# Kernel optimization log

Measured on AMD Instinct MI355X. Metric: run time of the kernel, lower is better.

Reference implementation:

```python
import jax, jax.numpy as jnp
import numpy as np

N_GRAPHS = 512
NODES_PER_G = 200
EDGES_PER_G = 6400
N = N_GRAPHS * NODES_PER_G        # 102400 nodes
E = N_GRAPHS * EDGES_PER_G        # 3276800 edges
HID = 128
NCLS = 10


def _linear_params(key, fan_in, fan_out):
    # torch nn.Linear default init: U(-1/sqrt(fan_in), 1/sqrt(fan_in))
    s = 1.0 / np.sqrt(fan_in)
    kw, kb = jax.random.split(key)
    W = jax.random.uniform(kw, (fan_in, fan_out), minval=-s, maxval=s, dtype=jnp.float32)
    b = jax.random.uniform(kb, (fan_out,), minval=-s, maxval=s, dtype=jnp.float32)
    return W, b


def setup_inputs() -> dict:
    key = jax.random.key(0)
    ks = jax.random.split(key, 10)
    # edges are confined within each graph (DGL batched graph structure)
    g_off = (jnp.arange(E, dtype=jnp.int32) // EDGES_PER_G) * NODES_PER_G
    src = (g_off + jax.random.randint(ks[0], (E,), 0, NODES_PER_G)).astype(jnp.int32)
    dst = (g_off + jax.random.randint(ks[1], (E,), 0, NODES_PER_G)).astype(jnp.int32)
    W1, b1 = _linear_params(ks[2], 1, HID)
    W2, b2 = _linear_params(ks[3], HID, HID)
    Wa, ba = _linear_params(ks[4], HID, 512)
    Wb, bb = _linear_params(ks[5], 512, 1024)
    Wc, bc = _linear_params(ks[6], 1024, 1024)
    Wd, bd = _linear_params(ks[7], 1024, 512)
    We, be = _linear_params(ks[8], 512, NCLS)
    return dict(src=src, dst=dst, W1=W1, b1=b1, W2=W2, b2=b2,
                Wa=Wa, ba=ba, Wb=Wb, bb=bb, Wc=Wc, bc=bc,
                Wd=Wd, bd=bd, We=We, be=be)


def reference(src, dst, W1, b1, W2, b2, Wa, ba, Wb, bb, Wc, bc, Wd, bd, We, be):
    seg = jax.ops.segment_sum
    ones = jnp.ones((E,), jnp.float32)
    in_deg = seg(ones, dst, num_segments=N)    # [N]
    out_deg = seg(ones, src, num_segments=N)   # [N]
    # DGL GraphConv norm='both': degrees clamped to min 1
    inv_out = (1.0 / jnp.sqrt(jnp.maximum(out_deg, 1.0)))[:, None]
    inv_in = (1.0 / jnp.sqrt(jnp.maximum(in_deg, 1.0)))[:, None]

    def gconv(h, W, b):
        h = (h @ W) * inv_out                    # src-side normalize (weight applied first; same math)
        h = seg(h[src], dst, num_segments=N)     # gather + scatter-add aggregation
        return h * inv_in + b                    # dst-side normalize + bias

    h = in_deg[:, None]                          # input node features = in-degrees, [N,1]
    h = jax.nn.relu(gconv(h, W1, b1))
    h = jax.nn.relu(gconv(h, W2, b2))

    gid = jnp.arange(N, dtype=jnp.int32) // NODES_PER_G
    hg = seg(h, gid, num_segments=N_GRAPHS) / float(NODES_PER_G)  # mean readout, [G,HID]

    x = jax.nn.relu(hg @ Wa + ba)
    x = jax.nn.relu(x @ Wb + bb)
    x = jax.nn.relu(x @ Wc + bc)
    x = jax.nn.relu(x @ Wd + bd)
    return jax.nn.softmax(x @ We + be, axis=-1)  # nn.Softmax over class dim
```

## Files before the change

### kernel.cpp

```cpp
#include <hip/hip_runtime.h>
#include <stdint.h>

typedef unsigned short u16;
typedef unsigned int   u32;

#define NG   512
#define NPG  200
#define EPG  6400
#define NN   (NG*NPG)
#define NE_  (NG*EPG)
#define HID  128
#define KP   224
#define AQS  232
#define ZP   136
#define QCAP 2048

__device__ __forceinline__ float bf2f(u16 b){ u32 u = ((u32)b) << 16; return __builtin_bit_cast(float, u); }
__device__ __forceinline__ u16 f2bf(float f){
    u32 u = __builtin_bit_cast(u32, f);
    u = (u + 0x7FFFu + ((u >> 16) & 1u)) >> 16;
    return (u16)u;
}

typedef __attribute__((ext_vector_type(8))) short bf16x8;
typedef __attribute__((ext_vector_type(4))) float f32x4;

enum : int { cW1=0, cb1=128, cb2=256, cba=384, cbb=896, cbc=1920, cbd=2944, cWe=3456, cbe=8576, cEND=8586 };
enum : int { T_Wa=0, T_Wb=65536, T_Wc=589824, T_Wd=1638400, T_END=2162688 };

struct PrepIn { const void* p[14]; };

__global__ __launch_bounds__(256) void k_prep2(PrepIn in, float* __restrict__ canon,
                                               u16* __restrict__ W2T, u16* __restrict__ WTa,
                                               float* __restrict__ hg)
{
    __shared__ u16 tile[64][72];
    __shared__ int sflag;
    const int tid = threadIdx.x;
    if (tid < 64){
        const u16* wb = (const u16*)in.p[0];
        u16 a = wb[tid], b = wb[64 + tid];
        unsigned long long m1 = __ballot((int)((a >> 7) & 0xFF) >= 0x7F);
        unsigned long long m2 = __ballot((int)((b >> 7) & 0xFF) >= 0x7F);
        if (tid == 0) sflag = (__popcll(m1) + __popcll(m2) > 4) ? 1 : 0;
    }
    __syncthreads();
    const int f = sflag;
    const int bid = blockIdx.x;

    if (tid < 116){
        int j = bid*116 + tid;
        if (j < NG*HID) hg[j] = 0.f;
    }

    if (bid < 532){
        const void* s; u16* dst; int K, N, t, lgn;
        if      (bid < 4)  { t = bid;       s = in.p[2];  dst = W2T;        K = 128;  N = 128;  lgn = 1; }
        else if (bid < 20) { t = bid - 4;   s = in.p[4];  dst = WTa + T_Wa; K = 128;  N = 512;  lgn = 3; }
        else if (bid < 148){ t = bid - 20;  s = in.p[6];  dst = WTa + T_Wb; K = 512;  N = 1024; lgn = 4; }
        else if (bid < 404){ t = bid - 148; s = in.p[8];  dst = WTa + T_Wc; K = 1024; N = 1024; lgn = 4; }
        else               { t = bid - 404; s = in.p[10]; dst = WTa + T_Wd; K = 1024; N = 512;  lgn = 3; }
        const int k0 = (t >> lgn) * 64, n0 = (t & ((1 << lgn) - 1)) * 64;
        #pragma unroll
        for (int i = 0; i < 16; i++){
            int idx = i*256 + tid;
            int kk = idx >> 6, nn = idx & 63;
            int si = (k0 + kk)*N + n0 + nn;
            tile[nn][kk] = f ? f2bf(((const float*)s)[si]) : ((const u16*)s)[si];
        }
        __syncthreads();
        #pragma unroll
        for (int i = 0; i < 16; i++){
            int idx = i*256 + tid;
            int nn = idx >> 6, kk = idx & 63;
            dst[(size_t)(n0 + nn)*K + k0 + kk] = tile[nn][kk];
        }
    } else {
        int i = (bid - 532)*256 + tid;
        if (i < cEND){
            const void* s; int off;
            if      (i < 128) { s = in.p[0];  off = i; }
            else if (i < 256) { s = in.p[1];  off = i - 128; }
            else if (i < 384) { s = in.p[3];  off = i - 256; }
            else if (i < 896) { s = in.p[5];  off = i - 384; }
            else if (i < 1920){ s = in.p[7];  off = i - 896; }
            else if (i < 2944){ s = in.p[9];  off = i - 1920; }
            else if (i < 3456){ s = in.p[11]; off = i - 2944; }
            else if (i < 8576){ s = in.p[12]; off = i - 3456; }
            else              { s = in.p[13]; off = i - 8576; }
            canon[i] = f ? ((const float*)s)[off] : bf2f(((const u16*)s)[off]);
        }
    }
}

__global__ __launch_bounds__(256) void k_l1(
    const int* __restrict__ src, const int* __restrict__ dst,
    const float* __restrict__ W1, const float* __restrict__ b1,
    float* __restrict__ invInG, u16* __restrict__ h1sT,
    u32* __restrict__ edgeBuf, int* __restrict__ cntQ)
{
    __shared__ u16 srcL[EPG];
    __shared__ u16 dstL[EPG];
    __shared__ int degIn[NPG], degOut[NPG];
    __shared__ int qcur[4];
    __shared__ float sAgg4[4][NPG];
    __shared__ float sValL[NPG], iiL[NPG], ioL[NPG], tL[NPG];
    __shared__ float w1L[HID], b1L[HID];

    const int g = blockIdx.x, tid = threadIdx.x;

    if (tid < NPG){
        degIn[tid] = 0; degOut[tid] = 0;
        sAgg4[0][tid] = 0.f; sAgg4[1][tid] = 0.f; sAgg4[2][tid] = 0.f; sAgg4[3][tid] = 0.f;
    }
    if (tid < HID){ w1L[tid] = W1[tid]; b1L[tid] = b1[tid]; }
    if (tid < 4) qcur[tid] = 0;
    __syncthreads();

    const int ebase = g * EPG;
    #pragma unroll
    for (int i = 0; i < EPG/256; i++){
        int e = i*256 + tid;
        int s = src[ebase + e] - g*NPG;
        int d = dst[ebase + e] - g*NPG;
        srcL[e] = (u16)s; dstL[e] = (u16)d;
        atomicAdd(&degOut[s], 1);
        atomicAdd(&degIn[d], 1);
    }
    __syncthreads();

    if (tid < NPG){
        float ii = rsqrtf(fmaxf((float)degIn[tid], 1.f));
        float io = rsqrtf(fmaxf((float)degOut[tid], 1.f));
        iiL[tid] = ii; ioL[tid] = io;
        sValL[tid] = (float)degIn[tid] * io;
        invInG[g*NPG + tid] = ii;
    }
    __syncthreads();

    const int rep = tid & 3;
    #pragma unroll
    for (int i = 0; i < EPG/256; i++){
        int e = i*256 + tid;
        int s = srcL[e], d = dstL[e];
        atomicAdd(&sAgg4[rep][d], sValL[s]);
        int q = (d * 41) >> 11;
        int pos = atomicAdd(&qcur[q], 1);
        if (pos < QCAP)
            edgeBuf[((size_t)(g*4 + q))*QCAP + pos] = (u32)s | ((u32)(d - q*50) << 16);
    }
    __syncthreads();

    if (tid < 4) cntQ[g*4 + tid] = (qcur[tid] < QCAP) ? qcur[tid] : QCAP;
    if (tid < NPG)
        tL[tid] = (sAgg4[0][tid] + sAgg4[1][tid] + sAgg4[2][tid] + sAgg4[3][tid]) * iiL[tid];
    __syncthreads();

    const size_t base = (size_t)g * HID * KP;
    #pragma unroll 4
    for (int i = 0; i < HID*KP/256; i++){
        int idx = i*256 + tid;
        int c = idx / KP, v = idx - c*KP;
        u16 o = 0;
        if (v < NPG)
            o = f2bf(fmaxf(fmaf(tL[v], w1L[c], b1L[c]), 0.f) * ioL[v]);
        h1sT[base + idx] = o;
    }
}

__global__ __launch_bounds__(256, 5) void k_quarter(
    const u32* __restrict__ edgeBuf, const int* __restrict__ cntQ,
    const u16* __restrict__ h1sT, const u16* __restrict__ W2T,
    const float* __restrict__ invInG, const float* __restrict__ b2,
    float* __restrict__ hg)
{
    __shared__ __align__(16) u16 Aq[64*AQS];
    __shared__ float invInL[64];
    __shared__ float b2L[HID];
    __shared__ float poolL[HID];

    const int bid = blockIdx.x, tid = threadIdx.x;
    const int xcd = bid & 7, slot = bid >> 3;
    const int g = (slot >> 2) * 8 + xcd;
    const int q = slot & 3;
    u32* aq32 = (u32*)Aq;

    if (tid < HID){ b2L[tid] = b2[tid]; poolL[tid] = 0.f; }
    if (tid < 64) invInL[tid] = (tid < 50) ? invInG[g*NPG + q*50 + tid] : 0.f;

    uint4* a4 = (uint4*)Aq;
    #pragma unroll
    for (int i = 0; i < 8; i++){
        int idx = i*256 + tid;
        if (idx < 64*AQS/8) a4[idx] = make_uint4(0,0,0,0);
    }
    __syncthreads();

    const int cnt = cntQ[g*4 + q];
    const u32* eb = edgeBuf + (size_t)(g*4 + q) * QCAP;
    for (int i = tid; i < cnt; i += 256){
        u32 e = eb[i];
        int idx = (int)(e >> 16) * AQS + (int)(e & 0xFFFF);
        atomicAdd(&aq32[idx >> 1], 1u << (16*(idx & 1)));
    }
    __syncthreads();

    for (int i = tid; i < 64*AQS/2; i += 256){
        u32 wv = aq32[i];
        if (wv)
            aq32[i] = (u32)f2bf((float)(wv & 0xFFFFu)) | ((u32)f2bf((float)(wv >> 16)) << 16);
    }
    __syncthreads();

    const int w = tid >> 6, lane = tid & 63;
    const int wm = w >> 1, wn = w & 1;
    const int lr = lane & 15, quad = lane >> 4;
    const f32x4 fz = {0.f, 0.f, 0.f, 0.f};

    f32x4 acc[2][4];
    #pragma unroll
    for (int mi = 0; mi < 2; mi++)
        #pragma unroll
        for (int nt = 0; nt < 4; nt++) acc[mi][nt] = fz;
    {
        const u16* Bg = h1sT + (size_t)g * HID * KP + (size_t)(wn*64) * KP;
        bf16x8 br[3][4];
        #pragma unroll
        for (int nt = 0; nt < 4; nt++){
            br[0][nt] = *(const bf16x8*)&Bg[(nt*16 + lr)*KP + quad*8];
            br[1][nt] = *(const bf16x8*)&Bg[(nt*16 + lr)*KP + 32 + quad*8];
        }
        #pragma unroll
        for (int ks = 0; ks < 7; ks++){
            const int sl = ks % 3, pf = (ks + 2) % 3;
            if (ks + 2 < 7){
                #pragma unroll
                for (int nt = 0; nt < 4; nt++)
                    br[pf][nt] = *(const bf16x8*)&Bg[(nt*16 + lr)*KP + (ks+2)*32 + quad*8];
            }
            bf16x8 af[2];
            #pragma unroll
            for (int mi = 0; mi < 2; mi++)
                af[mi] = *(const bf16x8*)&Aq[((wm*2 + mi)*16 + lr)*AQS + ks*32 + quad*8];
            #pragma unroll
            for (int mi = 0; mi < 2; mi++)
                #pragma unroll
                for (int nt = 0; nt < 4; nt++)
                    acc[mi][nt] = __builtin_amdgcn_mfma_f32_16x16x32_bf16(
                        af[mi], br[sl][nt], acc[mi][nt], 0, 0, 0);
        }
    }
    __syncthreads();

    u16* Zq = Aq;
    #pragma unroll
    for (int mi = 0; mi < 2; mi++)
        #pragma unroll
        for (int nt = 0; nt < 4; nt++){
            int vq = (wm*2 + mi)*16 + quad*4;
            int c = wn*64 + nt*16 + lr;
            Zq[(vq+0)*ZP + c] = f2bf(acc[mi][nt][0]);
            Zq[(vq+1)*ZP + c] = f2bf(acc[mi][nt][1]);
            Zq[(vq+2)*ZP + c] = f2bf(acc[mi][nt][2]);
            Zq[(vq+3)*ZP + c] = f2bf(acc[mi][nt][3]);
        }
    __syncthreads();

    f32x4 acc2[2][4];
    #pragma unroll
    for (int mi = 0; mi < 2; mi++)
        #pragma unroll
        for (int nt = 0; nt < 4; nt++) acc2[mi][nt] = fz;
    {
        const u16* Wg = W2T + (size_t)(wn*64) * HID;
        bf16x8 bcur[4], bnxt[4];
        #pragma unroll
        for (int nt = 0; nt < 4; nt++)
            bcur[nt] = *(const bf16x8*)&Wg[(nt*16 + lr)*HID + quad*8];
        #pragma unroll
        for (int ks = 0; ks < 4; ks++){
            if (ks < 3){
                #pragma unroll
                for (int nt = 0; nt < 4; nt++)
                    bnxt[nt] = *(const bf16x8*)&Wg[(nt*16 + lr)*HID + (ks+1)*32 + quad*8];
            }
            bf16x8 za[2];
            #pragma unroll
            for (int mi = 0; mi < 2; mi++)
                za[mi] = *(const bf16x8*)&Zq[((wm*2 + mi)*16 + lr)*ZP + ks*32 + quad*8];
            #pragma unroll
            for (int mi = 0; mi < 2; mi++)
                #pragma unroll
                for (int nt = 0; nt < 4; nt++)
                    acc2[mi][nt] = __builtin_amdgcn_mfma_f32_16x16x32_bf16(
                        za[mi], bcur[nt], acc2[mi][nt], 0, 0, 0);
            #pragma unroll
            for (int nt = 0; nt < 4; nt++) bcur[nt] = bnxt[nt];
        }
    }

    #pragma unroll
    for (int mi = 0; mi < 2; mi++)
        #pragma unroll
        for (int nt = 0; nt < 4; nt++){
            int cout = wn*64 + nt*16 + lr;
            float s = 0.f;
            #pragma unroll
            for (int r = 0; r < 4; r++){
                int vq = (wm*2 + mi)*16 + quad*4 + r;
                if (vq < 50)
                    s += fmaxf(fmaf(acc2[mi][nt][r], invInL[vq], b2L[cout]), 0.f);
            }
            atomicAdd(&poolL[cout], s);
        }
    __syncthreads();
    if (tid < HID) atomicAdd(&hg[(size_t)g*HID + tid], poolL[tid] * (1.f / NPG));
}

template<int K, bool AF32>
__global__ __launch_bounds__(512) void k_mlp6(
    const void* __restrict__ Ahi_, const u16* __restrict__ Alo,
    const u16* __restrict__ WT, const float* __restrict__ bias,
    u16* __restrict__ Ohi, u16* __restrict__ Olo, int Nc)
{
    constexpr int ITERS = K / 64;
    __shared__ __align__(16) float red[32][36];

    const int tid = threadIdx.x;
    const int w = tid >> 6, lane = tid & 63;
    const int kz = w >> 2, wm = (w >> 1) & 1, wn = w & 1;
    const int lr = lane & 15, quad = lane >> 4;
    const int row0 = blockIdx.x * 32, col0 = blockIdx.y * 32;
    const int m = row0 + wm*16 + lr;
    const int n = col0 + wn*16 + lr;
    const int k0 = kz * (K/2);

    const float* Af = (const float*)Ahi_;
    const u16*   Ah = (const u16*)Ahi_;

    auto loadA = [&](int it, bf16x8& hi, bf16x8& lo){
        const int kk = k0 + it*32 + quad*8;
        if constexpr (AF32){
            float xs[8];
            *(float4*)&xs[0] = *(const float4*)&Af[(size_t)m*K + kk];
            *(float4*)&xs[4] = *(const float4*)&Af[(size_t)m*K + kk + 4];
            #pragma unroll
            for (int j = 0; j < 8; j++){
                u16 hh = f2bf(xs[j]);
                hi[j] = (short)hh;
                lo[j] = (short)f2bf(xs[j] - bf2f(hh));
            }
        } else {
            hi = *(const bf16x8*)&Ah[(size_t)m*K + kk];
            lo = *(const bf16x8*)&Alo[(size_t)m*K + kk];
        }
    };

    const f32x4 fz = {0.f, 0.f, 0.f, 0.f};
    f32x4 acc = fz;
    bf16x8 hi[3], lo[3], bb[3];
    loadA(0, hi[0], lo[0]);
    bb[0] = *(const bf16x8*)&WT[(size_t)n*K + k0 + quad*8];
    if (ITERS > 1){
        loadA(1, hi[1], lo[1]);
        bb[1] = *(const bf16x8*)&WT[(size_t)n*K + k0 + 32 + quad*8];
    }
    #pragma unroll
    for (int it = 0; it < ITERS; it++){
        const int sl = it % 3, pf = (it + 2) % 3;
        if (it + 2 < ITERS){
            loadA(it+2, hi[pf], lo[pf]);
            bb[pf] = *(const bf16x8*)&WT[(size_t)n*K + k0 + (it+2)*32 + quad*8];
        }
        acc = __builtin_amdgcn_mfma_f32_16x16x32_bf16(hi[sl], bb[sl], acc, 0, 0, 0);
        acc = __builtin_amdgcn_mfma_f32_16x16x32_bf16(lo[sl], bb[sl], acc, 0, 0, 0);
    }

    if (kz == 1){
        #pragma unroll
        for (int r = 0; r < 4; r++)
            red[wm*16 + quad*4 + r][wn*16 + lr] = acc[r];
    }
    __syncthreads();
    if (kz == 0){
        #pragma unroll
        for (int r = 0; r < 4; r++){
            int rr = wm*16 + quad*4 + r;
            int cc = wn*16 + lr;
            float v = acc[r] + red[rr][cc] + bias[col0 + cc];
            v = fmaxf(v, 0.f);
            u16 hh = f2bf(v);
            size_t go = (size_t)(row0 + rr) * Nc + col0 + cc;
            Ohi[go] = hh;
            Olo[go] = f2bf(v - bf2f(hh));
        }
    }
}

__global__ __launch_bounds__(64) void k_head(
    const u16* __restrict__ Xhi, const u16* __restrict__ Xlo,
    const float* __restrict__ We, const float* __restrict__ be,
    void* __restrict__ out, const u16* __restrict__ w1bits)
{
    const int g = blockIdx.x, lane = threadIdx.x;
    u16 a = w1bits[lane], b = w1bits[64 + lane];
    unsigned long long m1 = __ballot((int)((a >> 7) & 0xFF) >= 0x7F);
    unsigned long long m2 = __ballot((int)((b >> 7) & 0xFF) >= 0x7F);
    const int f = (__popcll(m1) + __popcll(m2) > 4) ? 1 : 0;

    float part[10];
    #pragma unroll
    for (int c = 0; c < 10; c++) part[c] = 0.f;
    for (int k = lane; k < 512; k += 64){
        float x = bf2f(Xhi[(size_t)g*512 + k]) + bf2f(Xlo[(size_t)g*512 + k]);
        #pragma unroll
        for (int c = 0; c < 10; c++) part[c] = fmaf(x, We[k*10 + c], part[c]);
    }
    #pragma unroll
    for (int c = 0; c < 10; c++){
        float v = part[c];
        for (int off = 32; off > 0; off >>= 1) v += __shfl_down(v, off);
        part[c] = v;
    }
    if (lane == 0){
        #pragma unroll
        for (int c = 0; c < 10; c++) part[c] += be[c];
        float m = part[0];
        #pragma unroll
        for (int c = 1; c < 10; c++) m = fmaxf(m, part[c]);
        float e[10], s = 0.f;
        #pragma unroll
        for (int c = 0; c < 10; c++){ e[c] = __expf(part[c] - m); s += e[c]; }
        float inv = 1.f / s;
        #pragma unroll
        for (int c = 0; c < 10; c++){
            float p = e[c] * inv;
            if (f) ((float*)out)[g*10 + c] = p;
            else   ((u16*)out)[g*10 + c]  = f2bf(p);
        }
    }
}

extern "C" void kernel_launch(void* const* d_in, const int* in_sizes, int n_in,
                              void* d_out, int out_size, void* d_ws, size_t ws_size,
                              hipStream_t stream)
{
    const int* src = (const int*)d_in[0];
    const int* dst = (const int*)d_in[1];

    char* ws = (char*)d_ws;
    size_t o = 0;
    float* canon    = (float*)(ws + o); o += ((size_t)cEND * 4 + 15) & ~(size_t)15;
    u16*   W2T      = (u16*)  (ws + o); o += (size_t)HID * HID * 2;
    u16*   WTa      = (u16*)  (ws + o); o += ((size_t)T_END * 2 + 15) & ~(size_t)15;
    float* invIn    = (float*)(ws + o); o += (size_t)NN * 4;
    u32*   edgeBuf  = (u32*)  (ws + o); o += (size_t)NG * 4 * QCAP * 4;
    int*   cntQ     = (int*)  (ws + o); o += (size_t)NG * 4 * 4;
    u16*   h1sT     = (u16*)  (ws + o); o += (size_t)NG * HID * KP * 2;
    float* hg       = (float*)(ws + o); o += (size_t)NG * HID * 4;
    u16*   X1hi     = (u16*)  (ws + o); o += (size_t)NG * 512 * 2;
    u16*   X1lo     = (u16*)  (ws + o); o += (size_t)NG * 512 * 2;
    u16*   X2hi     = (u16*)  (ws + o); o += (size_t)NG * 1024 * 2;
    u16*   X2lo     = (u16*)  (ws + o); o += (size_t)NG * 1024 * 2;
    u16*   X3hi     = (u16*)  (ws + o); o += (size_t)NG * 1024 * 2;
    u16*   X3lo     = (u16*)  (ws + o); o += (size_t)NG * 1024 * 2;
    u16*   X4hi     = (u16*)  (ws + o); o += (size_t)NG * 512 * 2;
    u16*   X4lo     = (u16*)  (ws + o); o += (size_t)NG * 512 * 2;
    (void)ws_size; (void)in_sizes; (void)n_in; (void)out_size;

    PrepIn pin;
    for (int i = 0; i < 14; i++) pin.p[i] = d_in[2 + i];
    k_prep2<<<dim3(566), dim3(256), 0, stream>>>(pin, canon, W2T, WTa, hg);

    const float *W1 = canon+cW1, *b1 = canon+cb1, *b2 = canon+cb2;
    const float *ba = canon+cba, *bb = canon+cbb, *bc = canon+cbc, *bd = canon+cbd;
    const float *We = canon+cWe, *be = canon+cbe;

    k_l1<<<dim3(NG), dim3(256), 0, stream>>>(
        src, dst, W1, b1, invIn, h1sT, edgeBuf, cntQ);

    k_quarter<<<dim3(NG*4), dim3(256), 0, stream>>>(
        edgeBuf, cntQ, h1sT, W2T, invIn, b2, hg);

    k_mlp6<128,  true ><<<dim3(16, 16), dim3(512), 0, stream>>>(hg,   nullptr, WTa + T_Wa, ba, X1hi, X1lo, 512);
    k_mlp6<512,  false><<<dim3(16, 32), dim3(512), 0, stream>>>(X1hi, X1lo,    WTa + T_Wb, bb, X2hi, X2lo, 1024);
    k_mlp6<1024, false><<<dim3(16, 32), dim3(512), 0, stream>>>(X2hi, X2lo,    WTa + T_Wc, bc, X3hi, X3lo, 1024);
    k_mlp6<1024, false><<<dim3(16, 16), dim3(512), 0, stream>>>(X3hi, X3lo,    WTa + T_Wd, bd, X4hi, X4lo, 512);

    k_head<<<dim3(NG), dim3(64), 0, stream>>>(X4hi, X4lo, We, be, d_out, (const u16*)d_in[2]);
}
```

Baseline: 261.7 us.

## Aggregate queue atomics per wave, vectorize h1 stores, prefetch B panel early

In k_l1, each wave now ballots on the target quarter and does one shared atomicAdd per quarter instead of one per edge. The h1sT writes are packed into 16-byte stores of 8 bf16 values. In k_quarter, the whole B panel (28 bf16x8 registers) is loaded from global memory at kernel start, so its latency overlaps the LDS zeroing and adjacency build. Launch bounds are lowered from 5 to 3 blocks per SM to make room for the extra registers, which reduces occupancy.

```diff
diff --git a/kernel.cpp b/kernel.cpp
--- a/kernel.cpp
+++ b/kernel.cpp
@@ -3,6 +3,7 @@
 
 typedef unsigned short u16;
 typedef unsigned int   u32;
+typedef unsigned long long u64;
 
 #define NG   512
 #define NPG  200
@@ -40,8 +41,8 @@
     if (tid < 64){
         const u16* wb = (const u16*)in.p[0];
         u16 a = wb[tid], b = wb[64 + tid];
-        unsigned long long m1 = __ballot((int)((a >> 7) & 0xFF) >= 0x7F);
-        unsigned long long m2 = __ballot((int)((b >> 7) & 0xFF) >= 0x7F);
+        u64 m1 = __ballot((int)((a >> 7) & 0xFF) >= 0x7F);
+        u64 m2 = __ballot((int)((b >> 7) & 0xFF) >= 0x7F);
         if (tid == 0) sflag = (__popcll(m1) + __popcll(m2) > 4) ? 1 : 0;
     }
     __syncthreads();
@@ -108,6 +109,7 @@
     __shared__ float w1L[HID], b1L[HID];
 
     const int g = blockIdx.x, tid = threadIdx.x;
+    const int lane = tid & 63;
 
     if (tid < NPG){
         degIn[tid] = 0; degOut[tid] = 0;
@@ -145,7 +147,14 @@
         int s = srcL[e], d = dstL[e];
         atomicAdd(&sAgg4[rep][d], sValL[s]);
         int q = (d * 41) >> 11;
-        int pos = atomicAdd(&qcur[q], 1);
+        u64 m0 = __ballot(q == 0), m1 = __ballot(q == 1);
+        u64 m2 = __ballot(q == 2), m3 = __ballot(q == 3);
+        u64 mine = (q == 0) ? m0 : (q == 1) ? m1 : (q == 2) ? m2 : m3;
+        int lead = __ffsll((unsigned long long)mine) - 1;
+        int base = 0;
+        if (lane == lead) base = atomicAdd(&qcur[q], __popcll(mine));
+        base = __shfl(base, lead);
+        int pos = base + __popcll(mine & ((1ull << lane) - 1ull));
         if (pos < QCAP)
             edgeBuf[((size_t)(g*4 + q))*QCAP + pos] = (u32)s | ((u32)(d - q*50) << 16);
     }
@@ -156,19 +165,27 @@
         tL[tid] = (sAgg4[0][tid] + sAgg4[1][tid] + sAgg4[2][tid] + sAgg4[3][tid]) * iiL[tid];
     __syncthreads();
 
-    const size_t base = (size_t)g * HID * KP;
-    #pragma unroll 4
-    for (int i = 0; i < HID*KP/256; i++){
+    uint4* hv = (uint4*)(h1sT + (size_t)g * HID * KP);
+    #pragma unroll 2
+    for (int i = 0; i < HID*KP/8/256; i++){
         int idx = i*256 + tid;
-        int c = idx / KP, v = idx - c*KP;
-        u16 o = 0;
-        if (v < NPG)
-            o = f2bf(fmaxf(fmaf(tL[v], w1L[c], b1L[c]), 0.f) * ioL[v]);
-        h1sT[base + idx] = o;
-    }
-}
-
-__global__ __launch_bounds__(256, 5) void k_quarter(
+        int c = idx / 28;
+        int v0 = (idx - c*28) * 8;
+        float wc = w1L[c], bc = b1L[c];
+        u16 ov[8];
+        #pragma unroll
+        for (int j = 0; j < 8; j++){
+            int v = v0 + j;
+            ov[j] = (v < NPG) ? f2bf(fmaxf(fmaf(tL[v], wc, bc), 0.f) * ioL[v]) : (u16)0;
+        }
+        hv[idx] = make_uint4((u32)ov[0] | ((u32)ov[1] << 16),
+                             (u32)ov[2] | ((u32)ov[3] << 16),
+                             (u32)ov[4] | ((u32)ov[5] << 16),
+                             (u32)ov[6] | ((u32)ov[7] << 16));
+    }
+}
+
+__global__ __launch_bounds__(256, 3) void k_quarter(
     const u32* __restrict__ edgeBuf, const int* __restrict__ cntQ,
     const u16* __restrict__ h1sT, const u16* __restrict__ W2T,
     const float* __restrict__ invInG, const float* __restrict__ b2,
@@ -185,6 +202,20 @@
     const int q = slot & 3;
     u32* aq32 = (u32*)Aq;
 
+    const int w = tid >> 6, lane = tid & 63;
+    const int wm = w >> 1, wn = w & 1;
+    const int lr = lane & 15, quad = lane >> 4;
+
+    bf16x8 bpan[7][4];
+    {
+        const u16* Bg = h1sT + (size_t)g * HID * KP + (size_t)(wn*64) * KP;
+        #pragma unroll
+        for (int ks = 0; ks < 7; ks++)
+            #pragma unroll
+            for (int nt = 0; nt < 4; nt++)
+                bpan[ks][nt] = *(const bf16x8*)&Bg[(nt*16 + lr)*KP + ks*32 + quad*8];
+    }
+
     if (tid < HID){ b2L[tid] = b2[tid]; poolL[tid] = 0.f; }
     if (tid < 64) invInL[tid] = (tid < 50) ? invInG[g*NPG + q*50 + tid] : 0.f;
 
@@ -212,9 +243,6 @@
     }
     __syncthreads();
 
-    const int w = tid >> 6, lane = tid & 63;
-    const int wm = w >> 1, wn = w & 1;
-    const int lr = lane & 15, quad = lane >> 4;
     const f32x4 fz = {0.f, 0.f, 0.f, 0.f};
 
     f32x4 acc[2][4];
@@ -222,33 +250,18 @@
     for (int mi = 0; mi < 2; mi++)
         #pragma unroll
         for (int nt = 0; nt < 4; nt++) acc[mi][nt] = fz;
-    {
-        const u16* Bg = h1sT + (size_t)g * HID * KP + (size_t)(wn*64) * KP;
-        bf16x8 br[3][4];
-        #pragma unroll
-        for (int nt = 0; nt < 4; nt++){
-            br[0][nt] = *(const bf16x8*)&Bg[(nt*16 + lr)*KP + quad*8];
-            br[1][nt] = *(const bf16x8*)&Bg[(nt*16 + lr)*KP + 32 + quad*8];
-        }
-        #pragma unroll
-        for (int ks = 0; ks < 7; ks++){
-            const int sl = ks % 3, pf = (ks + 2) % 3;
-            if (ks + 2 < 7){
-                #pragma unroll
-                for (int nt = 0; nt < 4; nt++)
-                    br[pf][nt] = *(const bf16x8*)&Bg[(nt*16 + lr)*KP + (ks+2)*32 + quad*8];
-            }
-            bf16x8 af[2];
-            #pragma unroll
-            for (int mi = 0; mi < 2; mi++)
-                af[mi] = *(const bf16x8*)&Aq[((wm*2 + mi)*16 + lr)*AQS + ks*32 + quad*8];
-            #pragma unroll
-            for (int mi = 0; mi < 2; mi++)
-                #pragma unroll
-                for (int nt = 0; nt < 4; nt++)
-                    acc[mi][nt] = __builtin_amdgcn_mfma_f32_16x16x32_bf16(
-                        af[mi], br[sl][nt], acc[mi][nt], 0, 0, 0);
-        }
+    #pragma unroll
+    for (int ks = 0; ks < 7; ks++){
+        bf16x8 af[2];
+        #pragma unroll
+        for (int mi = 0; mi < 2; mi++)
+            af[mi] = *(const bf16x8*)&Aq[((wm*2 + mi)*16 + lr)*AQS + ks*32 + quad*8];
+        #pragma unroll
+        for (int mi = 0; mi < 2; mi++)
+            #pragma unroll
+            for (int nt = 0; nt < 4; nt++)
+                acc[mi][nt] = __builtin_amdgcn_mfma_f32_16x16x32_bf16(
+                    af[mi], bpan[ks][nt], acc[mi][nt], 0, 0, 0);
     }
     __syncthreads();
 
@@ -404,8 +417,8 @@
 {
     const int g = blockIdx.x, lane = threadIdx.x;
     u16 a = w1bits[lane], b = w1bits[64 + lane];
-    unsigned long long m1 = __ballot((int)((a >> 7) & 0xFF) >= 0x7F);
-    unsigned long long m2 = __ballot((int)((b >> 7) & 0xFF) >= 0x7F);
+    u64 m1 = __ballot((int)((a >> 7) & 0xFF) >= 0x7F);
+    u64 m2 = __ballot((int)((b >> 7) & 0xFF) >= 0x7F);
     const int f = (__popcll(m1) + __popcll(m2) > 4) ? 1 : 0;
 
     float part[10];
```

Measured after the change: 269.2 us. 1.03x slower.
